# Kernel tuning notes

Measured on AMD Instinct MI355X. Metric: run time of the kernel, lower is better.

The kernel has to match this reference:

```python
import jax, jax.numpy as jnp
import numpy as np

B, T, E, H, A, V = 32, 128, 256, 512, 256, 32000
S_SRC, S_CUE = 64, 64
OUT_IN = E + 2 * H + 2 * H  # emb + rnn_out + knowledge + src_ctx + cue_ctx (memory_size=H)
NEG = -1e9


def setup_inputs() -> dict:
    key = jax.random.key(0)
    ks = jax.random.split(key, 20)
    s = lambda k, sh: (jax.random.normal(k, sh) / np.sqrt(sh[0])).astype(jnp.float32)
    inp = {}
    inp['tokens'] = jax.random.randint(ks[0], (B, T), 0, V)
    inp['lengths'] = jax.random.randint(ks[1], (B,), 1, T + 1)
    inp['hidden0'] = jax.random.normal(ks[2], (B, H)) * 0.1
    inp['knowledge'] = jax.random.normal(ks[3], (B, H)) * 0.1
    inp['src_mem'] = jax.random.normal(ks[4], (B, S_SRC, H)) * 0.1
    inp['src_lengths'] = jax.random.randint(ks[5], (B,), 1, S_SRC + 1)
    inp['cue_mem'] = jax.random.normal(ks[6], (B, S_CUE, H)) * 0.1
    inp['cue_lengths'] = jax.random.randint(ks[7], (B,), 1, S_CUE + 1)
    # parameters
    inp['emb'] = jax.random.normal(ks[8], (V, E)) * 0.02
    inp['w_ih'] = s(ks[9], (E, 3 * H)); inp['w_hh'] = s(ks[10], (H, 3 * H))
    inp['b_ih'] = jnp.zeros((3 * H,)); inp['b_hh'] = jnp.zeros((3 * H,))
    Q = E + 2 * H
    inp['src_wq'] = s(ks[11], (Q, A)); inp['src_bq'] = jnp.zeros((A,))
    inp['src_wm'] = s(ks[12], (H, A)); inp['src_v'] = s(ks[13], (A,))
    inp['cue_wq'] = s(ks[14], (Q, A)); inp['cue_bq'] = jnp.zeros((A,))
    inp['cue_wm'] = s(ks[15], (H, A)); inp['cue_v'] = s(ks[16], (A,))
    inp['w_out1'] = s(ks[17], (OUT_IN, H)); inp['b_out1'] = jnp.zeros((H,))
    inp['w_out2'] = s(ks[18], (H, V)); inp['b_out2'] = jnp.zeros((V,))
    return inp


def _mlp_attn(q, mk, mem, wq, bq, v, mask):
    # q: (B,Q), mk = mem@wm precomputed: (B,S,A), mem: (B,S,H), mask: (B,S) True=valid
    scores = jnp.einsum('bsa,a->bs', jnp.tanh((q @ wq + bq)[:, None, :] + mk), v)
    scores = jnp.where(mask, scores, NEG)
    w = jax.nn.softmax(scores, axis=-1)
    return jnp.einsum('bs,bsh->bh', w, mem)


def reference(tokens, lengths, hidden0, knowledge, src_mem, src_lengths, cue_mem,
              cue_lengths, emb, w_ih, w_hh, b_ih, b_hh, src_wq, src_bq, src_wm,
              src_v, cue_wq, cue_bq, cue_wm, cue_v, w_out1, b_out1, w_out2, b_out2):
    x_all = emb[tokens]                                   # (B,T,E) teacher-forced embeddings
    valid = jnp.arange(T)[None, :] < lengths[:, None]     # (B,T)
    src_mask = jnp.arange(S_SRC)[None, :] < src_lengths[:, None]
    cue_mask = jnp.arange(S_CUE)[None, :] < cue_lengths[:, None]
    src_mk = src_mem @ src_wm                             # (B,S,A) hoisted memory projection
    cue_mk = cue_mem @ cue_wm

    def step(h, xs):
        x, vm = xs                                        # (B,E), (B,)
        gi = x @ w_ih + b_ih
        gh = h @ w_hh + b_hh
        i_r, i_z, i_n = jnp.split(gi, 3, axis=-1)
        h_r, h_z, h_n = jnp.split(gh, 3, axis=-1)
        r = jax.nn.sigmoid(i_r + h_r)
        z = jax.nn.sigmoid(i_z + h_z)
        n = jnp.tanh(i_n + r * h_n)
        h_new = (1.0 - z) * n + z * h                     # torch GRU cell
        q = jnp.concatenate([x, h, knowledge], axis=-1)   # query uses OLD hidden (as in source)
        src_ctx = _mlp_attn(q, src_mk, src_mem, src_wq, src_bq, src_v, src_mask)
        cue_ctx = _mlp_attn(q, cue_mk, cue_mem, cue_wq, cue_bq, cue_v, cue_mask)
        out_in = jnp.concatenate([x, h_new, knowledge, src_ctx, cue_ctx], axis=-1)
        vmc = vm[:, None]
        h_next = jnp.where(vmc, h_new, h)                 # only valid rows advance (length-sorted loop)
        return h_next, (jnp.where(vmc, out_in, 0.0), jnp.where(vmc, h_new, 0.0))

    h_final, (out_inputs, hid_mem) = jax.lax.scan(
        step, hidden0, (x_all.transpose(1, 0, 2), valid.T))
    out_inputs = out_inputs.transpose(1, 0, 2)            # (B,T,OUT_IN)
    hidden_memory = hid_mem.transpose(1, 0, 2)            # (B,T,H)
    logits = (out_inputs @ w_out1 + b_out1) @ w_out2 + b_out2
    log_probs = jax.nn.log_softmax(logits, axis=-1)       # (B,T,V)
    return log_probs, hidden_memory, h_final
```

## Files before the change

kernel.cpp:

```cpp
#include <hip/hip_runtime.h>

typedef unsigned int uint;
typedef unsigned short ushort;
using short8 = __attribute__((ext_vector_type(8))) short;
using f32x4  = __attribute__((ext_vector_type(4))) float;

#define DEVFN __device__ __forceinline__

constexpr int B_ = 32, T_ = 128, E_ = 256, H_ = 512, A_ = 256, V_ = 32000, S_ = 64;
constexpr int G3_ = 3 * H_;
constexpr int OUTIN_ = E_ + 4 * H_;
constexpr int M_ = B_ * T_;

DEVFN ushort f2b(float f) {
  uint u = __float_as_uint(f);
  u += 0x7fffu + ((u >> 16) & 1u);
  return (ushort)(u >> 16);
}
DEVFN float b2f(ushort b) { return __uint_as_float(((uint)b) << 16); }
DEVFN float sigmoid_f(float x) { return 1.f / (1.f + __expf(-x)); }
DEVFN float tanh_f(float x) { float e = __expf(2.f * x); return 1.f - 2.f / (e + 1.f); }
DEVFN f32x4 MFMA16(short8 a, short8 b, f32x4 c) {
  return __builtin_amdgcn_mfma_f32_16x16x32_bf16(a, b, c, 0, 0, 0);
}

DEVFN void trans_tile(const float* in, ushort* out, int R, int C, int bx, int by,
                      int tid, char* smem) {
  ushort (*tile)[65] = (ushort(*)[65])smem;
  int c0 = bx * 64, r0 = by * 64;
  int tx = tid & 63, ty = tid >> 6;
#pragma unroll
  for (int k = 0; k < 16; k++) {
    int i = ty + k * 4;
    int r = r0 + i, c = c0 + tx;
    if (r < R && c < C) tile[tx][i] = f2b(in[(size_t)r * C + c]);
  }
  __syncthreads();
#pragma unroll
  for (int k = 0; k < 16; k++) {
    int j = ty + k * 4;
    int c = c0 + j, r = r0 + tx;
    if (r < R && c < C) out[(size_t)c * R + r] = tile[j][tx];
  }
  __syncthreads();
}

struct PArgs {
  const float *w_ih, *src_wq, *cue_wq, *src_wm, *cue_wm, *src_mem, *cue_mem, *h0, *emb;
  const int* tokens;
  ushort *wiht, *wqxts, *wqxtc, *wqht2, *wmts, *wmtc, *membs, *membc, *hpb, *xbf;
};

__global__ __launch_bounds__(256) void prologue_k(PArgs P) {
  __shared__ __align__(16) char smem[8448];
  const int j = blockIdx.x, tid = threadIdx.x;
  if (j < 96) {
    trans_tile(P.w_ih, P.wiht, E_, G3_, j % 24, j / 24, tid, smem);
  } else if (j < 112) {
    int q = j - 96;  trans_tile(P.src_wq, P.wqxts, E_, A_, q & 3, q >> 2, tid, smem);
  } else if (j < 144) {
    int q = j - 112; trans_tile(P.src_wq + (size_t)E_ * A_, P.wqht2, H_, A_, q & 3, q >> 2, tid, smem);
  } else if (j < 160) {
    int q = j - 144; trans_tile(P.cue_wq, P.wqxtc, E_, A_, q & 3, q >> 2, tid, smem);
  } else if (j < 192) {
    int q = j - 160; trans_tile(P.cue_wq + (size_t)E_ * A_, P.wqht2 + (size_t)256 * H_, H_, A_, q & 3, q >> 2, tid, smem);
  } else if (j < 224) {
    int q = j - 192; trans_tile(P.src_wm, P.wmts, H_, A_, q & 3, q >> 2, tid, smem);
  } else if (j < 256) {
    int q = j - 224; trans_tile(P.cue_wm, P.wmtc, H_, A_, q & 3, q >> 2, tid, smem);
  } else if (j < 512) {
    int base = (j - 256) * 4096;
#pragma unroll
    for (int i = 0; i < 16; i++) { int g = base + i * 256 + tid; P.membs[g] = f2b(P.src_mem[g]); }
  } else if (j < 768) {
    int base = (j - 512) * 4096;
#pragma unroll
    for (int i = 0; i < 16; i++) { int g = base + i * 256 + tid; P.membc[g] = f2b(P.cue_mem[g]); }
  } else if (j < 832) {
    int g = (j - 768) * 256 + tid;
    P.hpb[g] = f2b(P.h0[g]);
  } else {
    int r = j - 832;
    int t = r >> 5, b = r & 31;
    int tok = P.tokens[b * T_ + t];
    P.xbf[(size_t)r * E_ + tid] = f2b(P.emb[(size_t)tok * E_ + tid]);
  }
}
constexpr int NPRO = 4928;

template <int OUTBF, int PERM, int HASBIAS>
__global__ __launch_bounds__(256) void gemm_bt(const ushort* __restrict__ Ag,
                                               const ushort* __restrict__ Btg,
                                               const float* __restrict__ bias,
                                               void* __restrict__ Cg, int M, int N, int K) {
  __shared__ __align__(16) ushort Ash[128][40];
  __shared__ __align__(16) ushort Bsh[128][40];
  const int nbx = gridDim.x;
  const int nwg = nbx * gridDim.y;
  const int lin = blockIdx.y * nbx + blockIdx.x;
  const int cpx = nwg >> 3;
  const int swz = (lin & 7) * cpx + (lin >> 3);
  const int m0 = (swz / nbx) * 128, n0 = (swz % nbx) * 128;
  const int tid = threadIdx.x;
  const int wave = tid >> 6, lane = tid & 63, lr = lane & 15, lg = lane >> 4;
  const int wr = wave >> 1, wc = wave & 1;
  f32x4 acc[4][4] = {};
  for (int kk = 0; kk < K; kk += 32) {
    {
      int r = tid >> 2, q = tid & 3;
      *(short8*)&Ash[r][q * 8] = *(const short8*)&Ag[(size_t)(m0 + r) * K + kk + q * 8];
      *(short8*)&Bsh[r][q * 8] = *(const short8*)&Btg[(size_t)(n0 + r) * K + kk + q * 8];
      r += 64;
      *(short8*)&Ash[r][q * 8] = *(const short8*)&Ag[(size_t)(m0 + r) * K + kk + q * 8];
      *(short8*)&Bsh[r][q * 8] = *(const short8*)&Btg[(size_t)(n0 + r) * K + kk + q * 8];
    }
    __syncthreads();
    short8 af[4], bfr[4];
#pragma unroll
    for (int mi = 0; mi < 4; mi++) af[mi] = *(const short8*)&Ash[wr * 64 + mi * 16 + lr][lg * 8];
#pragma unroll
    for (int ni = 0; ni < 4; ni++) bfr[ni] = *(const short8*)&Bsh[wc * 64 + ni * 16 + lr][lg * 8];
#pragma unroll
    for (int mi = 0; mi < 4; mi++)
#pragma unroll
      for (int ni = 0; ni < 4; ni++)
        acc[mi][ni] = MFMA16(af[mi], bfr[ni], acc[mi][ni]);
    __syncthreads();
  }
#pragma unroll
  for (int mi = 0; mi < 4; mi++)
#pragma unroll
    for (int ni = 0; ni < 4; ni++) {
      int col = n0 + wc * 64 + ni * 16 + lr;
      float bv = HASBIAS ? bias[col] : 0.f;
#pragma unroll
      for (int r = 0; r < 4; r++) {
        int row = m0 + wr * 64 + mi * 16 + lg * 4 + r;
        int orow = PERM ? ((row & 31) << 7) + (row >> 5) : row;
        float v = acc[mi][ni][r] + bv;
        if (OUTBF == 1)      ((ushort*)Cg)[(size_t)orow * N + col] = f2b(v);
        else if (OUTBF == 2) ((ushort*)Cg)[(size_t)orow * 2 * N + col] = f2b(v);
        else                 ((float*)Cg)[(size_t)orow * N + col] = v;
      }
    }
}

struct FArgs {
  const float *w_hh, *b_hh, *gi, *h0;
  const int* lengths;
  ushort* hpb;
  float *hidmem, *hfinal;
  uint* flags;
  const float *w_out1, *w_out2, *knowledge, *src_wq, *src_bq, *cue_wq, *cue_bq;
  ushort *wo1t, *wo2t;
  float *kqs, *kqc;
  const ushort *xbf, *wqxts, *wqxtc, *membs, *membc, *wmts, *wmtc;
  float *qxks, *qxkc, *mks, *mkc;
};

DEVFN void scan_body(const FArgs& P, int wg, int tid, char* smem) {
  ushort (*pk)[16][16] = (ushort(*)[16][16])smem;
  const int c0 = wg * 16;
  const int wave = tid >> 6, lane = tid & 63, lr = lane & 15, lg = lane >> 4;
  const int c = c0 + lr;

  short8 wf0[16], wf1[16], wf2[16];
#pragma unroll
  for (int kk = 0; kk < 16; kk++) {
    short8 v0, v1, v2;
#pragma unroll
    for (int i = 0; i < 8; i++) {
      int k = kk * 32 + lg * 8 + i;
      v0[i] = (short)f2b(P.w_hh[(size_t)k * G3_ + 0 * H_ + c]);
      v1[i] = (short)f2b(P.w_hh[(size_t)k * G3_ + 1 * H_ + c]);
      v2[i] = (short)f2b(P.w_hh[(size_t)k * G3_ + 2 * H_ + c]);
    }
    wf0[kk] = v0; wf1[kk] = v1; wf2[kk] = v2;
  }
  const float bh0 = P.b_hh[c], bh1 = P.b_hh[H_ + c], bh2 = P.b_hh[2 * H_ + c];
  int len[4];
  float hp[4];
#pragma unroll
  for (int r = 0; r < 4; r++) {
    int bt = 16 * wave + lg * 4 + r;
    len[r] = P.lengths[bt];
    hp[r] = P.h0[(size_t)bt * H_ + c];
  }
  const uint fidx = ((uint)(lane & 31) * 2 + (uint)wave) * 32;

#pragma unroll 1
  for (int t = 0; t < T_; t++) {
    float g0[4], g1[4], g2[4];
#pragma unroll
    for (int r = 0; r < 4; r++) {
      int bt = 16 * wave + lg * 4 + r;
      const float* gr = P.gi + (size_t)(t * 32 + bt) * G3_ + c;
      g0[r] = gr[0]; g1[r] = gr[H_]; g2[r] = gr[2 * H_];
    }
    if (t > 0) {
      while (true) {
        uint f = __hip_atomic_load(&P.flags[fidx], __ATOMIC_RELAXED, __HIP_MEMORY_SCOPE_AGENT);
        if (__all((int)(f >= (uint)t))) break;
        __builtin_amdgcn_s_sleep(1);
      }
    }
    asm volatile("" ::: "memory");

    const ushort* Sb = P.hpb + (size_t)t * (B_ * H_);
    const int rowA = 16 * wave + lr;
    f32x4 a0 = {}, a1 = {}, a2 = {};
#pragma unroll
    for (int kk = 0; kk < 16; kk++) {
      short8 av = *(const short8*)(Sb + rowA * H_ + kk * 32 + lg * 8);
      a0 = MFMA16(av, wf0[kk], a0);
      a1 = MFMA16(av, wf1[kk], a1);
      a2 = MFMA16(av, wf2[kk], a2);
    }

    ushort* Un16 = P.hpb + (size_t)(t + 1) * (B_ * H_);
    float hmv[4];
#pragma unroll
    for (int r = 0; r < 4; r++) {
      float rr = sigmoid_f(g0[r] + a0[r] + bh0);
      float zz = sigmoid_f(g1[r] + a1[r] + bh1);
      float nn = tanh_f(g2[r] + rr * (a2[r] + bh2));
      float hv = (1.f - zz) * nn + zz * hp[r];
      bool valid = t < len[r];
      float hx = valid ? hv : hp[r];
      hp[r] = hx;
      hmv[r] = valid ? hv : 0.f;
      pk[wave][lg * 4 + r][lr] = f2b(hx);
    }
    if (lane < 32) {
      int row = lane >> 1, half = lane & 1;
      short8 v = *(const short8*)&pk[wave][row][half * 8];
      ushort* gp = Un16 + ((size_t)(16 * wave + row) * H_ + c0 + half * 8);
      asm volatile("global_store_dwordx4 %0, %1, off sc1" :: "v"(gp), "v"(v) : "memory");
    }
    asm volatile("s_waitcnt vmcnt(0)" ::: "memory");
    if (lane == 0)
      __hip_atomic_store(&P.flags[(wg * 2 + wave) * 32], (uint)(t + 1),
                         __ATOMIC_RELAXED, __HIP_MEMORY_SCOPE_AGENT);
#pragma unroll
    for (int r = 0; r < 4; r++) {
      int bt = 16 * wave + lg * 4 + r;
      P.hidmem[((size_t)bt * T_ + t) * H_ + c] = hmv[r];
    }
  }
#pragma unroll
  for (int r = 0; r < 4; r++) {
    int bt = 16 * wave + lg * 4 + r;
    P.hfinal[(size_t)bt * H_ + c] = hp[r];
  }
}

DEVFN void kq_job(const float* knowledge, const float* wq, const float* bq,
                  float* kq, int b, int tid) {
  const float* kn = knowledge + b * H_;
  float s = 0.f;
  for (int h = 0; h < H_; h++) s += kn[h] * wq[(size_t)(E_ + H_ + h) * A_ + tid];
  kq[b * A_ + tid] = s + bq[tid];
}

DEVFN void gemm_tile(const ushort* Ag, const ushort* Btg, float* Cg,
                     int N, int K, int m0, int n0, int tid, char* smem) {
  ushort (*Ash)[40] = (ushort(*)[40])smem;
  ushort (*Bsh)[40] = (ushort(*)[40])(smem + 10240);
  const int wave = tid >> 6, lane = tid & 63, lr = lane & 15, lg = lane >> 4;
  const int wr = wave >> 1, wc = wave & 1;
  f32x4 acc[4][4] = {};
  for (int kk = 0; kk < K; kk += 32) {
    {
      int r = tid >> 2, q = tid & 3;
      *(short8*)&Ash[r][q * 8] = *(const short8*)&Ag[(size_t)(m0 + r) * K + kk + q * 8];
      *(short8*)&Bsh[r][q * 8] = *(const short8*)&Btg[(size_t)(n0 + r) * K + kk + q * 8];
      r += 64;
      *(short8*)&Ash[r][q * 8] = *(const short8*)&Ag[(size_t)(m0 + r) * K + kk + q * 8];
      *(short8*)&Bsh[r][q * 8] = *(const short8*)&Btg[(size_t)(n0 + r) * K + kk + q * 8];
    }
    __syncthreads();
    short8 af[4], bfr[4];
#pragma unroll
    for (int mi = 0; mi < 4; mi++) af[mi] = *(const short8*)&Ash[wr * 64 + mi * 16 + lr][lg * 8];
#pragma unroll
    for (int ni = 0; ni < 4; ni++) bfr[ni] = *(const short8*)&Bsh[wc * 64 + ni * 16 + lr][lg * 8];
#pragma unroll
    for (int mi = 0; mi < 4; mi++)
#pragma unroll
      for (int ni = 0; ni < 4; ni++)
        acc[mi][ni] = MFMA16(af[mi], bfr[ni], acc[mi][ni]);
    __syncthreads();
  }
#pragma unroll
  for (int mi = 0; mi < 4; mi++)
#pragma unroll
    for (int ni = 0; ni < 4; ni++) {
      int col = n0 + wc * 64 + ni * 16 + lr;
#pragma unroll
      for (int r = 0; r < 4; r++) {
        int row = m0 + wr * 64 + mi * 16 + lg * 4 + r;
        Cg[(size_t)row * N + col] = acc[mi][ni][r];
      }
    }
}

constexpr int NJOB = 288 + 4000 + 64 + 128 + 64;

__global__ __launch_bounds__(256, 1) void scanfused_k(FArgs P) {
  __shared__ __align__(16) char smem[20480];
  const int bid = blockIdx.x, tid = threadIdx.x;
  if (bid < 32) {
    if (tid < 128) scan_body(P, bid, tid, smem);
    return;
  }
  for (int j = bid - 32; j < NJOB; j += 224) {
    if (j < 288) {
      trans_tile(P.w_out1, P.wo1t, OUTIN_, H_, j & 7, j >> 3, tid, smem);
    } else if (j < 4288) {
      int q = j - 288;
      trans_tile(P.w_out2, P.wo2t, H_, V_, q % 500, q / 500, tid, smem);
    } else if (j < 4352) {
      int q = j - 4288;
      if (q < 32) kq_job(P.knowledge, P.src_wq, P.src_bq, P.kqs, q, tid);
      else        kq_job(P.knowledge, P.cue_wq, P.cue_bq, P.kqc, q - 32, tid);
    } else if (j < 4480) {
      int q = j - 4352;
      int mat = q >> 6; q &= 63;
      gemm_tile(P.xbf, mat ? P.wqxtc : P.wqxts, mat ? P.qxkc : P.qxks,
                A_, E_, (q >> 1) * 128, (q & 1) * 128, tid, smem);
    } else {
      int q = j - 4480;
      int mat = q >> 5; q &= 31;
      gemm_tile(mat ? P.membc : P.membs, mat ? P.wmtc : P.wmts, mat ? P.mkc : P.mks,
                A_, H_, (q >> 1) * 128, (q & 1) * 128, tid, smem);
    }
  }
}

struct AArgs {
  const float* qxk[2];
  const float* kq[2];
  const float* mk[2];
  const ushort* memb[2];
  const float* vvec[2];
  const int* slen[2];
  float* ctx[2];
  const float* qh2;
};

__global__ __launch_bounds__(256) void attn2_k(AArgs P) {
  __shared__ float qf[A_], vv[A_], sc[S_];
  int bid = blockIdx.x;
  int mat = bid >> 12;
  int bx = bid & 4095;
  int b = bx >> 7, t = bx & 127;
  int row = t * B_ + b;
  int tid = threadIdx.x;
  qf[tid] = P.qxk[mat][(size_t)row * A_ + tid] +
            P.qh2[(size_t)row * 512 + mat * 256 + tid] + P.kq[mat][b * A_ + tid];
  vv[tid] = P.vvec[mat][tid];
  __syncthreads();
  int s = tid >> 2, q4 = tid & 3;
  const float* mkr = P.mk[mat] + ((size_t)(b * S_) + s) * A_;
  float part = 0.f;
#pragma unroll 4
  for (int i = 0; i < 64; i++) {
    int a = q4 + (i << 2);
    part += tanh_f(qf[a] + mkr[a]) * vv[a];
  }
  part += __shfl_xor(part, 1, 64);
  part += __shfl_xor(part, 2, 64);
  if (q4 == 0) sc[s] = part;
  __syncthreads();
  if (tid < S_) {
    float v = (tid < P.slen[mat][b]) ? sc[tid] : -1e9f;
    float mm = v;
    for (int off = 1; off < 64; off <<= 1) mm = fmaxf(mm, __shfl_xor(mm, off, 64));
    float e = __expf(v - mm);
    float ss = e;
    for (int off = 1; off < 64; off <<= 1) ss += __shfl_xor(ss, off, 64);
    sc[tid] = e / ss;
  }
  __syncthreads();
  float c0 = 0.f, c1 = 0.f;
  const ushort* mb = P.memb[mat] + (size_t)b * S_ * H_;
  for (int ss2 = 0; ss2 < S_; ss2++) {
    float w = sc[ss2];
    c0 += w * b2f(mb[ss2 * H_ + tid]);
    c1 += w * b2f(mb[ss2 * H_ + tid + 256]);
  }
  P.ctx[mat][(size_t)row * H_ + tid] = c0;
  P.ctx[mat][(size_t)row * H_ + tid + 256] = c1;
}

__global__ __launch_bounds__(256) void assemble_k(
    const ushort* __restrict__ xbf, const float* __restrict__ hm,
    const float* __restrict__ knowledge, const float* __restrict__ ctxs,
    const float* __restrict__ ctxc, const int* __restrict__ lengths,
    ushort* __restrict__ outin) {
  int r = blockIdx.x;
  int t = r >> 5, b = r & 31;
  bool valid = t < lengths[b];
  int tid = threadIdx.x;
  ushort* dst = outin + (size_t)r * OUTIN_;
#pragma unroll
  for (int kblk = 0; kblk < 9; kblk++) {
    int i = kblk * 256 + tid;
    ushort v;
    if (i < E_)               v = xbf[(size_t)r * E_ + i];
    else if (i < E_ + H_)     v = f2b(hm[((size_t)b * T_ + t) * H_ + i - E_]);
    else if (i < E_ + 2 * H_) v = f2b(knowledge[b * H_ + i - (E_ + H_)]);
    else if (i < E_ + 3 * H_) v = f2b(ctxs[(size_t)r * H_ + i - (E_ + 2 * H_)]);
    else                      v = f2b(ctxc[(size_t)r * H_ + i - (E_ + 3 * H_)]);
    dst[i] = valid ? v : (ushort)0;
  }
}

__global__ __launch_bounds__(256) void logsoftmax_k(float* __restrict__ logits) {
  __shared__ float redm[4], reds[4];
  float* row = logits + (size_t)blockIdx.x * V_;
  const short8* rg = (const short8*)row;
  const int tid = threadIdx.x;
  short8 buf[16];
  float m = -3.4e38f, s = 0.f;
#pragma unroll
  for (int k = 0; k < 16; k++) {
    int i = tid + k * 256;
    if (i < V_ / 8) {
      short8 v = rg[i];
      buf[k] = v;
      float f0 = b2f((ushort)v[0]), f1 = b2f((ushort)v[1]);
      float f2 = b2f((ushort)v[2]), f3 = b2f((ushort)v[3]);
      float f4 = b2f((ushort)v[4]), f5 = b2f((ushort)v[5]);
      float f6 = b2f((ushort)v[6]), f7 = b2f((ushort)v[7]);
      float vm = fmaxf(fmaxf(fmaxf(f0, f1), fmaxf(f2, f3)),
                       fmaxf(fmaxf(f4, f5), fmaxf(f6, f7)));
      float nm = fmaxf(m, vm);
      s = s * __expf(m - nm) + __expf(f0 - nm) + __expf(f1 - nm) + __expf(f2 - nm) +
          __expf(f3 - nm) + __expf(f4 - nm) + __expf(f5 - nm) + __expf(f6 - nm) +
          __expf(f7 - nm);
      m = nm;
    }
  }
  for (int off = 1; off < 64; off <<= 1) {
    float om = __shfl_xor(m, off, 64), os = __shfl_xor(s, off, 64);
    float nm = fmaxf(m, om);
    s = s * __expf(m - nm) + os * __expf(om - nm);
    m = nm;
  }
  if ((tid & 63) == 0) { redm[tid >> 6] = m; reds[tid >> 6] = s; }
  __syncthreads();
  float M = fmaxf(fmaxf(redm[0], redm[1]), fmaxf(redm[2], redm[3]));
  float S = reds[0] * __expf(redm[0] - M) + reds[1] * __expf(redm[1] - M) +
            reds[2] * __expf(redm[2] - M) + reds[3] * __expf(redm[3] - M);
  float lse = M + __logf(S);
  __syncthreads();
#pragma unroll
  for (int k = 0; k < 16; k++) {
    int i = tid + k * 256;
    if (i < V_ / 8) {
      short8 v = buf[k];
      float4 o0, o1;
      o0.x = b2f((ushort)v[0]) - lse; o0.y = b2f((ushort)v[1]) - lse;
      o0.z = b2f((ushort)v[2]) - lse; o0.w = b2f((ushort)v[3]) - lse;
      o1.x = b2f((ushort)v[4]) - lse; o1.y = b2f((ushort)v[5]) - lse;
      o1.z = b2f((ushort)v[6]) - lse; o1.w = b2f((ushort)v[7]) - lse;
      *(float4*)&row[i * 8] = o0;
      *(float4*)&row[i * 8 + 4] = o1;
    }
  }
}

extern "C" void kernel_launch(void* const* d_in, const int* in_sizes, int n_in,
                              void* d_out, int out_size, void* d_ws, size_t ws_size,
                              hipStream_t stream) {
  const int*   tokens    = (const int*)  d_in[0];
  const int*   lengths   = (const int*)  d_in[1];
  const float* hidden0   = (const float*)d_in[2];
  const float* knowledge = (const float*)d_in[3];
  const float* src_mem   = (const float*)d_in[4];
  const int*   src_len   = (const int*)  d_in[5];
  const float* cue_mem   = (const float*)d_in[6];
  const int*   cue_len   = (const int*)  d_in[7];
  const float* emb       = (const float*)d_in[8];
  const float* w_ih      = (const float*)d_in[9];
  const float* w_hh      = (const float*)d_in[10];
  const float* b_ih      = (const float*)d_in[11];
  const float* b_hh      = (const float*)d_in[12];
  const float* src_wq    = (const float*)d_in[13];
  const float* src_bq    = (const float*)d_in[14];
  const float* src_wm    = (const float*)d_in[15];
  const float* src_v     = (const float*)d_in[16];
  const float* cue_wq    = (const float*)d_in[17];
  const float* cue_bq    = (const float*)d_in[18];
  const float* cue_wm    = (const float*)d_in[19];
  const float* cue_v     = (const float*)d_in[20];
  const float* w_out1    = (const float*)d_in[21];
  const float* b_out1    = (const float*)d_in[22];
  const float* w_out2    = (const float*)d_in[23];
  const float* b_out2    = (const float*)d_in[24];

  float* out_lp = (float*)d_out;
  float* out_hm = out_lp + (size_t)M_ * V_;
  float* out_hf = out_hm + (size_t)M_ * H_;

  char* scb = (char*)d_out;
  size_t off = 0;
  auto alloc = [&](size_t bytes) -> void* {
    void* p = scb + off;
    off = (off + bytes + 255) & ~(size_t)255;
    return p;
  };
  float*  GI    = (float*) alloc((size_t)M_ * G3_ * 4);
  float*  QXKs  = (float*) alloc((size_t)M_ * A_ * 4);
  float*  QXKc  = (float*) alloc((size_t)M_ * A_ * 4);
  float*  QH2   = (float*) alloc((size_t)M_ * 512 * 4);
  float*  CTXs  = (float*) alloc((size_t)M_ * H_ * 4);
  float*  CTXc  = (float*) alloc((size_t)M_ * H_ * 4);
  ushort* OUTIN = (ushort*)alloc((size_t)M_ * OUTIN_ * 2);
  ushort* XBF   = (ushort*)alloc((size_t)M_ * E_ * 2);
  ushort* WIHT  = (ushort*)alloc((size_t)G3_ * E_ * 2);
  ushort* WQXTs = (ushort*)alloc((size_t)A_ * E_ * 2);
  ushort* WQXTc = (ushort*)alloc((size_t)A_ * E_ * 2);
  ushort* WQHT2 = (ushort*)alloc((size_t)512 * H_ * 2);
  ushort* WMTs  = (ushort*)alloc((size_t)A_ * H_ * 2);
  ushort* WMTc  = (ushort*)alloc((size_t)A_ * H_ * 2);
  ushort* WO1T  = (ushort*)alloc((size_t)H_ * OUTIN_ * 2);
  ushort* MEMBs = (ushort*)alloc((size_t)B_ * S_ * H_ * 2);
  ushort* MEMBc = (ushort*)alloc((size_t)B_ * S_ * H_ * 2);
  float*  MKs   = (float*) alloc((size_t)B_ * S_ * A_ * 4);
  float*  MKc   = (float*) alloc((size_t)B_ * S_ * A_ * 4);
  float*  KQs   = (float*) alloc((size_t)B_ * A_ * 4);
  float*  KQc   = (float*) alloc((size_t)B_ * A_ * 4);
  ushort* HPB   = (ushort*)alloc((size_t)(T_ + 1) * B_ * H_ * 2);

  uint* FLAGS = (uint*)d_ws;
  ushort* WO2T = (ushort*)((char*)d_ws + 8192);
  ushort* HID1 = (ushort*)((char*)d_ws + 8192 + (size_t)V_ * H_ * 2);

  dim3 blk(256);
  hipMemsetAsync(FLAGS, 0, 8192, stream);

  PArgs PP;
  PP.w_ih = w_ih; PP.src_wq = src_wq; PP.cue_wq = cue_wq;
  PP.src_wm = src_wm; PP.cue_wm = cue_wm;
  PP.src_mem = src_mem; PP.cue_mem = cue_mem; PP.h0 = hidden0; PP.emb = emb;
  PP.tokens = tokens;
  PP.wiht = WIHT; PP.wqxts = WQXTs; PP.wqxtc = WQXTc; PP.wqht2 = WQHT2;
  PP.wmts = WMTs; PP.wmtc = WMTc; PP.membs = MEMBs; PP.membc = MEMBc;
  PP.hpb = HPB; PP.xbf = XBF;
  prologue_k<<<dim3(NPRO), blk, 0, stream>>>(PP);

  gemm_bt<0, 0, 1><<<dim3(G3_ / 128, M_ / 128), blk, 0, stream>>>(XBF, WIHT, b_ih, GI, M_, G3_, E_);

  FArgs P;
  P.w_hh = w_hh; P.b_hh = b_hh; P.gi = GI; P.h0 = hidden0;
  P.lengths = lengths; P.hpb = HPB; P.hidmem = out_hm; P.hfinal = out_hf; P.flags = FLAGS;
  P.w_out1 = w_out1; P.w_out2 = w_out2; P.knowledge = knowledge;
  P.src_wq = src_wq; P.src_bq = src_bq; P.cue_wq = cue_wq; P.cue_bq = cue_bq;
  P.wo1t = WO1T; P.wo2t = WO2T; P.kqs = KQs; P.kqc = KQc;
  P.xbf = XBF; P.wqxts = WQXTs; P.wqxtc = WQXTc;
  P.membs = MEMBs; P.membc = MEMBc; P.wmts = WMTs; P.wmtc = WMTc;
  P.qxks = QXKs; P.qxkc = QXKc; P.mks = MKs; P.mkc = MKc;
  scanfused_k<<<dim3(256), blk, 0, stream>>>(P);

  gemm_bt<0, 0, 0><<<dim3(512 / 128, M_ / 128), blk, 0, stream>>>(HPB, WQHT2, nullptr, QH2, M_, 512, H_);

  AArgs AA;
  AA.qxk[0] = QXKs; AA.qxk[1] = QXKc;
  AA.kq[0] = KQs; AA.kq[1] = KQc;
  AA.mk[0] = MKs; AA.mk[1] = MKc;
  AA.memb[0] = MEMBs; AA.memb[1] = MEMBc;
  AA.vvec[0] = src_v; AA.vvec[1] = cue_v;
  AA.slen[0] = src_len; AA.slen[1] = cue_len;
  AA.ctx[0] = CTXs; AA.ctx[1] = CTXc;
  AA.qh2 = QH2;
  attn2_k<<<dim3(2 * M_), blk, 0, stream>>>(AA);

  assemble_k<<<M_, blk, 0, stream>>>(XBF, out_hm, knowledge, CTXs, CTXc, lengths, OUTIN);
  gemm_bt<1, 0, 1><<<dim3(H_ / 128, M_ / 128), blk, 0, stream>>>(OUTIN, WO1T, b_out1, HID1, M_, H_, OUTIN_);
  gemm_bt<2, 1, 1><<<dim3(V_ / 128, M_ / 128), blk, 0, stream>>>(HID1, WO2T, b_out2, out_lp, M_, V_, H_);
  logsoftmax_k<<<M_, blk, 0, stream>>>(out_lp);
}
```

Before: 1.312 ms.

## Fold GI GEMM into fused scan kernel and fuse assemble into hid1 GEMM

The input-gate GEMM (x @ w_ih) moves from a separate launch into the worker blocks of the fused scan kernel. It writes with sc1 stores and bumps a global counter, and the scan blocks spin on that counter before the recurrence starts. Separately, the assemble kernel and the first output GEMM are merged: hid1_k gathers embeddings, hidden states from HPB, knowledge and the attention contexts straight into shared-memory A tiles, converting to bf16 and masking rows on the fly. This removes one launch and the OUTIN materialisation round-trip, at the cost of the scan now waiting on GEMM tiles and the new kernel doing a more irregular gather.

Measured after the change: 1.315 ms. Within noise of the previous version (+0.2%).

```diff
diff --git a/kernel.cpp b/kernel.cpp
--- a/kernel.cpp
+++ b/kernel.cpp
@@ -138,23 +138,23 @@
         int row = m0 + wr * 64 + mi * 16 + lg * 4 + r;
         int orow = PERM ? ((row & 31) << 7) + (row >> 5) : row;
         float v = acc[mi][ni][r] + bv;
-        if (OUTBF == 1)      ((ushort*)Cg)[(size_t)orow * N + col] = f2b(v);
-        else if (OUTBF == 2) ((ushort*)Cg)[(size_t)orow * 2 * N + col] = f2b(v);
-        else                 ((float*)Cg)[(size_t)orow * N + col] = v;
+        if (OUTBF == 2) ((ushort*)Cg)[(size_t)orow * 2 * N + col] = f2b(v);
+        else            ((float*)Cg)[(size_t)orow * N + col] = v;
       }
     }
 }
 
 struct FArgs {
-  const float *w_hh, *b_hh, *gi, *h0;
+  const float *w_hh, *b_hh, *b_ih, *h0;
+  float* gi;
   const int* lengths;
   ushort* hpb;
   float *hidmem, *hfinal;
-  uint* flags;
+  uint *flags, *gicnt;
   const float *w_out1, *w_out2, *knowledge, *src_wq, *src_bq, *cue_wq, *cue_bq;
   ushort *wo1t, *wo2t;
   float *kqs, *kqc;
-  const ushort *xbf, *wqxts, *wqxtc, *membs, *membc, *wmts, *wmtc;
+  const ushort *xbf, *wiht, *wqxts, *wqxtc, *membs, *membc, *wmts, *wmtc;
   float *qxks, *qxkc, *mks, *mkc;
 };
 
@@ -187,6 +187,13 @@
     hp[r] = P.h0[(size_t)bt * H_ + c];
   }
   const uint fidx = ((uint)(lane & 31) * 2 + (uint)wave) * 32;
+
+  while (true) {
+    uint g = __hip_atomic_load(P.gicnt, __ATOMIC_RELAXED, __HIP_MEMORY_SCOPE_AGENT);
+    if (__all((int)(g >= 384u))) break;
+    __builtin_amdgcn_s_sleep(8);
+  }
+  asm volatile("" ::: "memory");
 
 #pragma unroll 1
   for (int t = 0; t < T_; t++) {
@@ -304,7 +311,56 @@
     }
 }
 
-constexpr int NJOB = 288 + 4000 + 64 + 128 + 64;
+DEVFN void gemm_tile_gi(const ushort* Ag, const ushort* Btg, const float* bias, float* Cg,
+                        int N, int K, int m0, int n0, int tid, char* smem, uint* gicnt) {
+  ushort (*Ash)[40] = (ushort(*)[40])smem;
+  ushort (*Bsh)[40] = (ushort(*)[40])(smem + 10240);
+  const int wave = tid >> 6, lane = tid & 63, lr = lane & 15, lg = lane >> 4;
+  const int wr = wave >> 1, wc = wave & 1;
+  f32x4 acc[4][4] = {};
+  for (int kk = 0; kk < K; kk += 32) {
+    {
+      int r = tid >> 2, q = tid & 3;
+      *(short8*)&Ash[r][q * 8] = *(const short8*)&Ag[(size_t)(m0 + r) * K + kk + q * 8];
+      *(short8*)&Bsh[r][q * 8] = *(const short8*)&Btg[(size_t)(n0 + r) * K + kk + q * 8];
+      r += 64;
+      *(short8*)&Ash[r][q * 8] = *(const short8*)&Ag[(size_t)(m0 + r) * K + kk + q * 8];
+      *(short8*)&Bsh[r][q * 8] = *(const short8*)&Btg[(size_t)(n0 + r) * K + kk + q * 8];
+    }
+    __syncthreads();
+    short8 af[4], bfr[4];
+#pragma unroll
+    for (int mi = 0; mi < 4; mi++) af[mi] = *(const short8*)&Ash[wr * 64 + mi * 16 + lr][lg * 8];
+#pragma unroll
+    for (int ni = 0; ni < 4; ni++) bfr[ni] = *(const short8*)&Bsh[wc * 64 + ni * 16 + lr][lg * 8];
+#pragma unroll
+    for (int mi = 0; mi < 4; mi++)
+#pragma unroll
+      for (int ni = 0; ni < 4; ni++)
+        acc[mi][ni] = MFMA16(af[mi], bfr[ni], acc[mi][ni]);
+    __syncthreads();
+  }
+#pragma unroll
+  for (int mi = 0; mi < 4; mi++)
+#pragma unroll
+    for (int ni = 0; ni < 4; ni++) {
+      int col = n0 + wc * 64 + ni * 16 + lr;
+      float bv = bias[col];
+#pragma unroll
+      for (int r = 0; r < 4; r++) {
+        int row = m0 + wr * 64 + mi * 16 + lg * 4 + r;
+        float v = acc[mi][ni][r] + bv;
+        float* gp = &Cg[(size_t)row * N + col];
+        asm volatile("global_store_dword %0, %1, off sc1" :: "v"(gp), "v"(v) : "memory");
+      }
+    }
+  asm volatile("s_waitcnt vmcnt(0)" ::: "memory");
+  __syncthreads();
+  if (tid == 0)
+    __hip_atomic_fetch_add(gicnt, 1u, __ATOMIC_RELAXED, __HIP_MEMORY_SCOPE_AGENT);
+}
+
+constexpr int NJOB = 384 + 288 + 4000 + 64 + 128 + 64;
 
 __global__ __launch_bounds__(256, 1) void scanfused_k(FArgs P) {
   __shared__ __align__(16) char smem[20480];
@@ -314,22 +370,26 @@
     return;
   }
   for (int j = bid - 32; j < NJOB; j += 224) {
-    if (j < 288) {
-      trans_tile(P.w_out1, P.wo1t, OUTIN_, H_, j & 7, j >> 3, tid, smem);
-    } else if (j < 4288) {
-      int q = j - 288;
+    if (j < 384) {
+      gemm_tile_gi(P.xbf, P.wiht, P.b_ih, P.gi, G3_, E_,
+                   (j / 12) * 128, (j % 12) * 128, tid, smem, P.gicnt);
+    } else if (j < 672) {
+      int q = j - 384;
+      trans_tile(P.w_out1, P.wo1t, OUTIN_, H_, q & 7, q >> 3, tid, smem);
+    } else if (j < 4672) {
+      int q = j - 672;
       trans_tile(P.w_out2, P.wo2t, H_, V_, q % 500, q / 500, tid, smem);
-    } else if (j < 4352) {
-      int q = j - 4288;
+    } else if (j < 4736) {
+      int q = j - 4672;
       if (q < 32) kq_job(P.knowledge, P.src_wq, P.src_bq, P.kqs, q, tid);
       else        kq_job(P.knowledge, P.cue_wq, P.cue_bq, P.kqc, q - 32, tid);
-    } else if (j < 4480) {
-      int q = j - 4352;
+    } else if (j < 4864) {
+      int q = j - 4736;
       int mat = q >> 6; q &= 63;
       gemm_tile(P.xbf, mat ? P.wqxtc : P.wqxts, mat ? P.qxkc : P.qxks,
                 A_, E_, (q >> 1) * 128, (q & 1) * 128, tid, smem);
     } else {
-      int q = j - 4480;
+      int q = j - 4864;
       int mat = q >> 5; q &= 31;
       gemm_tile(mat ? P.membc : P.membs, mat ? P.wmtc : P.wmts, mat ? P.mkc : P.mks,
                 A_, H_, (q >> 1) * 128, (q & 1) * 128, tid, smem);
@@ -393,27 +453,81 @@
   P.ctx[mat][(size_t)row * H_ + tid + 256] = c1;
 }
 
-__global__ __launch_bounds__(256) void assemble_k(
-    const ushort* __restrict__ xbf, const float* __restrict__ hm,
-    const float* __restrict__ knowledge, const float* __restrict__ ctxs,
-    const float* __restrict__ ctxc, const int* __restrict__ lengths,
-    ushort* __restrict__ outin) {
-  int r = blockIdx.x;
-  int t = r >> 5, b = r & 31;
-  bool valid = t < lengths[b];
-  int tid = threadIdx.x;
-  ushort* dst = outin + (size_t)r * OUTIN_;
-#pragma unroll
-  for (int kblk = 0; kblk < 9; kblk++) {
-    int i = kblk * 256 + tid;
-    ushort v;
-    if (i < E_)               v = xbf[(size_t)r * E_ + i];
-    else if (i < E_ + H_)     v = f2b(hm[((size_t)b * T_ + t) * H_ + i - E_]);
-    else if (i < E_ + 2 * H_) v = f2b(knowledge[b * H_ + i - (E_ + H_)]);
-    else if (i < E_ + 3 * H_) v = f2b(ctxs[(size_t)r * H_ + i - (E_ + 2 * H_)]);
-    else                      v = f2b(ctxc[(size_t)r * H_ + i - (E_ + 3 * H_)]);
-    dst[i] = valid ? v : (ushort)0;
-  }
+struct HArgs {
+  const ushort *xbf, *hpb, *wo1t;
+  const float *knowledge, *ctxs, *ctxc, *b_out1;
+  const int* lengths;
+  ushort* hid1;
+};
+
+__global__ __launch_bounds__(256) void hid1_k(HArgs P) {
+  __shared__ __align__(16) ushort Ash[128][40];
+  __shared__ __align__(16) ushort Bsh[128][40];
+  const int nbx = gridDim.x;
+  const int nwg = nbx * gridDim.y;
+  const int lin = blockIdx.y * nbx + blockIdx.x;
+  const int cpx = nwg >> 3;
+  const int swz = (lin & 7) * cpx + (lin >> 3);
+  const int m0 = (swz / nbx) * 128, n0 = (swz % nbx) * 128;
+  const int tid = threadIdx.x;
+  const int wave = tid >> 6, lane = tid & 63, lr = lane & 15, lg = lane >> 4;
+  const int wr = wave >> 1, wc = wave & 1;
+  const short8 ZZ = {0, 0, 0, 0, 0, 0, 0, 0};
+  f32x4 acc[4][4] = {};
+  for (int kk = 0; kk < OUTIN_; kk += 32) {
+#pragma unroll
+    for (int half = 0; half < 2; half++) {
+      int rr = (tid >> 2) + half * 64;
+      int q = tid & 3;
+      int r = m0 + rr;
+      int t = r >> 5, b = r & 31;
+      bool valid = t < P.lengths[b];
+      int i0 = kk + q * 8;
+      short8 v;
+      if (kk < 256) {
+        v = *(const short8*)&P.xbf[(size_t)r * E_ + i0];
+      } else if (kk < 768) {
+        v = *(const short8*)&P.hpb[((size_t)(t + 1) * B_ + b) * H_ + (i0 - 256)];
+      } else {
+        const float* src = (kk < 1280) ? &P.knowledge[(size_t)b * H_ + (i0 - 768)]
+                         : (kk < 1792) ? &P.ctxs[(size_t)r * H_ + (i0 - 1280)]
+                                       : &P.ctxc[(size_t)r * H_ + (i0 - 1792)];
+        float4 f0 = *(const float4*)src;
+        float4 f1 = *(const float4*)(src + 4);
+        v[0] = (short)f2b(f0.x); v[1] = (short)f2b(f0.y);
+        v[2] = (short)f2b(f0.z); v[3] = (short)f2b(f0.w);
+        v[4] = (short)f2b(f1.x); v[5] = (short)f2b(f1.y);
+        v[6] = (short)f2b(f1.z); v[7] = (short)f2b(f1.w);
+      }
+      v = valid ? v : ZZ;
+      *(short8*)&Ash[rr][q * 8] = v;
+      *(short8*)&Bsh[rr][q * 8] = *(const short8*)&P.wo1t[(size_t)(n0 + rr) * OUTIN_ + kk + q * 8];
+    }
+    __syncthreads();
+    short8 af[4], bfr[4];
+#pragma unroll
+    for (int mi = 0; mi < 4; mi++) af[mi] = *(const short8*)&Ash[wr * 64 + mi * 16 + lr][lg * 8];
+#pragma unroll
+    for (int ni = 0; ni < 4; ni++) bfr[ni] = *(const short8*)&Bsh[wc * 64 + ni * 16 + lr][lg * 8];
+#pragma unroll
+    for (int mi = 0; mi < 4; mi++)
+#pragma unroll
+      for (int ni = 0; ni < 4; ni++)
+        acc[mi][ni] = MFMA16(af[mi], bfr[ni], acc[mi][ni]);
+    __syncthreads();
+  }
+#pragma unroll
+  for (int mi = 0; mi < 4; mi++)
+#pragma unroll
+    for (int ni = 0; ni < 4; ni++) {
+      int col = n0 + wc * 64 + ni * 16 + lr;
+      float bv = P.b_out1[col];
+#pragma unroll
+      for (int r = 0; r < 4; r++) {
+        int row = m0 + wr * 64 + mi * 16 + lg * 4 + r;
+        P.hid1[(size_t)row * H_ + col] = f2b(acc[mi][ni][r] + bv);
+      }
+    }
 }
 
 __global__ __launch_bounds__(256) void logsoftmax_k(float* __restrict__ logits) {
@@ -517,7 +631,6 @@
   float*  QH2   = (float*) alloc((size_t)M_ * 512 * 4);
   float*  CTXs  = (float*) alloc((size_t)M_ * H_ * 4);
   float*  CTXc  = (float*) alloc((size_t)M_ * H_ * 4);
-  ushort* OUTIN = (ushort*)alloc((size_t)M_ * OUTIN_ * 2);
   ushort* XBF   = (ushort*)alloc((size_t)M_ * E_ * 2);
   ushort* WIHT  = (ushort*)alloc((size_t)G3_ * E_ * 2);
   ushort* WQXTs = (ushort*)alloc((size_t)A_ * E_ * 2);
@@ -535,11 +648,12 @@
   ushort* HPB   = (ushort*)alloc((size_t)(T_ + 1) * B_ * H_ * 2);
 
   uint* FLAGS = (uint*)d_ws;
-  ushort* WO2T = (ushort*)((char*)d_ws + 8192);
-  ushort* HID1 = (ushort*)((char*)d_ws + 8192 + (size_t)V_ * H_ * 2);
+  uint* GICNT = (uint*)((char*)d_ws + 8192);
+  ushort* WO2T = (ushort*)((char*)d_ws + 16384);
+  ushort* HID1 = (ushort*)((char*)d_ws + 16384 + (size_t)V_ * H_ * 2);
 
   dim3 blk(256);
-  hipMemsetAsync(FLAGS, 0, 8192, stream);
+  hipMemsetAsync(d_ws, 0, 16384, stream);
 
   PArgs PP;
   PP.w_ih = w_ih; PP.src_wq = src_wq; PP.cue_wq = cue_wq;
@@ -551,15 +665,14 @@
   PP.hpb = HPB; PP.xbf = XBF;
   prologue_k<<<dim3(NPRO), blk, 0, stream>>>(PP);
 
-  gemm_bt<0, 0, 1><<<dim3(G3_ / 128, M_ / 128), blk, 0, stream>>>(XBF, WIHT, b_ih, GI, M_, G3_, E_);
-
   FArgs P;
-  P.w_hh = w_hh; P.b_hh = b_hh; P.gi = GI; P.h0 = hidden0;
-  P.lengths = lengths; P.hpb = HPB; P.hidmem = out_hm; P.hfinal = out_hf; P.flags = FLAGS;
+  P.w_hh = w_hh; P.b_hh = b_hh; P.b_ih = b_ih; P.h0 = hidden0; P.gi = GI;
+  P.lengths = lengths; P.hpb = HPB; P.hidmem = out_hm; P.hfinal = out_hf;
+  P.flags = FLAGS; P.gicnt = GICNT;
   P.w_out1 = w_out1; P.w_out2 = w_out2; P.knowledge = knowledge;
   P.src_wq = src_wq; P.src_bq = src_bq; P.cue_wq = cue_wq; P.cue_bq = cue_bq;
   P.wo1t = WO1T; P.wo2t = WO2T; P.kqs = KQs; P.kqc = KQc;
-  P.xbf = XBF; P.wqxts = WQXTs; P.wqxtc = WQXTc;
+  P.xbf = XBF; P.wiht = WIHT; P.wqxts = WQXTs; P.wqxtc = WQXTc;
   P.membs = MEMBs; P.membc = MEMBc; P.wmts = WMTs; P.wmtc = WMTc;
   P.qxks = QXKs; P.qxkc = QXKc; P.mks = MKs; P.mkc = MKc;
   scanfused_k<<<dim3(256), blk, 0, stream>>>(P);
@@ -577,8 +690,12 @@
   AA.qh2 = QH2;
   attn2_k<<<dim3(2 * M_), blk, 0, stream>>>(AA);
 
-  assemble_k<<<M_, blk, 0, stream>>>(XBF, out_hm, knowledge, CTXs, CTXc, lengths, OUTIN);
-  gemm_bt<1, 0, 1><<<dim3(H_ / 128, M_ / 128), blk, 0, stream>>>(OUTIN, WO1T, b_out1, HID1, M_, H_, OUTIN_);
+  HArgs HH;
+  HH.xbf = XBF; HH.hpb = HPB; HH.wo1t = WO1T;
+  HH.knowledge = knowledge; HH.ctxs = CTXs; HH.ctxc = CTXc; HH.b_out1 = b_out1;
+  HH.lengths = lengths; HH.hid1 = HID1;
+  hid1_k<<<dim3(H_ / 128, M_ / 128), blk, 0, stream>>>(HH);
+
   gemm_bt<2, 1, 1><<<dim3(V_ / 128, M_ / 128), blk, 0, stream>>>(HID1, WO2T, b_out2, out_lp, M_, V_, H_);
   logsoftmax_k<<<M_, blk, 0, stream>>>(out_lp);
 }
```
